# Kernel tuning notes

Hardware: AMD Instinct MI355X
Metric: run time of the kernel (lower is better)

## Reference

```python
import jax, jax.numpy as jnp
import numpy as np

B, N, H = 4096, 64, 256

def setup_inputs() -> dict:
    key = jax.random.key(0)
    ks = jax.random.split(key, 6)
    scale = 1.0 / np.sqrt(H)
    return {
        "s_t": jax.random.normal(ks[0], (B, H), dtype=jnp.float32),
        "h": jax.random.normal(ks[1], (1, N, H), dtype=jnp.float32) * scale,
        "w": jax.random.normal(ks[2], (1, N, H), dtype=jnp.float32) * scale,
        "U_w": jax.random.normal(ks[3], (H, H), dtype=jnp.float32) * scale,
        "V_w": jax.random.normal(ks[4], (H, H), dtype=jnp.float32) * scale,
        "W_w": jax.random.normal(ks[5], (H, H), dtype=jnp.float32) * scale,
        "prelu_a": jnp.full((1,), 0.25, dtype=jnp.float32),
    }

def _prelu(x, a):
    return jnp.where(x >= 0, x, a * x)

def reference(s_t, h, w, U_w, V_w, W_w, prelu_a):
    # gate: (h + w) @ s_t^T  -> [B, N]
    g = jax.nn.sigmoid(jnp.einsum('onh,bh->bn', h + w, s_t))[..., None]  # [B,N,1]
    # candidate: U(h) + V(w) + W(s_t), broadcast [1,N,H] + [B,1,H] -> [B,N,H]
    cand = _prelu(
        jnp.einsum('onh,kh->onk', h, U_w)
        + jnp.einsum('onh,kh->onk', w, V_w)
        + (s_t @ W_w.T)[:, None, :],
        prelu_a,
    )
    h_new = h + g * cand  # [B,N,H]
    h_new = h_new / jnp.linalg.norm(h_new, axis=2, keepdims=True)
    return h_new
```

## Files before the change

kernel.cpp:

```cpp
#include <hip/hip_runtime.h>
#include <hip/hip_bf16.h>

#define BATCH 4096
#define NMEM  64
#define HDIM  256
#define MROWS 320

typedef __attribute__((ext_vector_type(8))) short short8;
typedef __attribute__((ext_vector_type(4))) float floatx4;

__device__ __forceinline__ float bf2f(unsigned short u) {
    union { unsigned int i; float f; } v; v.i = ((unsigned int)u) << 16; return v.f;
}
__device__ __forceinline__ unsigned short f2bf(float f) {
    union { float f; unsigned int i; } v; v.f = f;
    unsigned int x = v.i;
    return (unsigned short)((x + 0x7FFFu + ((x >> 16) & 1u)) >> 16);
}
__device__ __forceinline__ short8 pack_bf16x8(float4 f0, float4 f1) {
    short8 a;
    a[0] = (short)f2bf(f0.x); a[1] = (short)f2bf(f0.y);
    a[2] = (short)f2bf(f0.z); a[3] = (short)f2bf(f0.w);
    a[4] = (short)f2bf(f1.x); a[5] = (short)f2bf(f1.y);
    a[6] = (short)f2bf(f1.z); a[7] = (short)f2bf(f1.w);
    return a;
}

__global__ __launch_bounds__(256) void prep_kernel(
    const float* __restrict__ h,
    const float* __restrict__ w,
    const float* __restrict__ U_w,
    const float* __restrict__ V_w,
    const float* __restrict__ W_w,
    unsigned short* __restrict__ M,
    unsigned short* __restrict__ A)
{
    const int bid = blockIdx.x;
    const int t   = threadIdx.x;
    if (bid < 16) {
        const int wv   = t >> 6;
        const int lane = t & 63;
        const int m = lane & 15;
        const int q = lane >> 4;
        const int j0 = bid * 16;

        const float* ah = h   + (size_t)(wv * 16 + m) * HDIM;
        const float* aw = w   + (size_t)(wv * 16 + m) * HDIM;
        const float* bu = U_w + (size_t)(j0 + m) * HDIM;
        const float* bv = V_w + (size_t)(j0 + m) * HDIM;

        floatx4 acc = {0.f, 0.f, 0.f, 0.f};
        #pragma unroll
        for (int ks = 0; ks < 16; ++ks) {
            const float* asrc = (ks < 8) ? ah : aw;
            const float* bsrc = (ks < 8) ? bu : bv;
            const int off = (ks & 7) * 32 + q * 8;
            float4 a0 = *(const float4*)(asrc + off);
            float4 a1 = *(const float4*)(asrc + off + 4);
            float4 b0 = *(const float4*)(bsrc + off);
            float4 b1 = *(const float4*)(bsrc + off + 4);
            acc = __builtin_amdgcn_mfma_f32_16x16x32_bf16(
                pack_bf16x8(a0, a1), pack_bf16x8(b0, b1), acc, 0, 0, 0);
        }
        #pragma unroll
        for (int r = 0; r < 4; ++r)
            A[(size_t)(wv * 16 + q * 4 + r) * HDIM + j0 + m] = f2bf(acc[r]);
    } else {
        const int r0 = (bid - 16) * 20;
        for (int rr = 0; rr < 20; ++rr) {
            const int r = r0 + rr;
            float v;
            if (r < 256) v = W_w[(size_t)r * HDIM + t];
            else         v = h[(size_t)(r - 256) * HDIM + t] + w[(size_t)(r - 256) * HDIM + t];
            M[(size_t)r * HDIM + t] = f2bf(v);
        }
    }
}

__global__ __launch_bounds__(256) void gemm_kernel(
    const float* __restrict__ s_t,
    const unsigned short* __restrict__ M,
    float* __restrict__ Call)
{
    const int b0   = blockIdx.x * 16;
    const int wave = threadIdx.x >> 6;
    const int lane = threadIdx.x & 63;
    const int m = lane & 15;
    const int q = lane >> 4;

    const float* arow = s_t + (size_t)(b0 + m) * HDIM;
    short8 afrag[8];
    #pragma unroll
    for (int ks = 0; ks < 8; ++ks) {
        const int base = ks * 32 + q * 8;
        afrag[ks] = pack_bf16x8(*(const float4*)(arow + base),
                                *(const float4*)(arow + base + 4));
    }

    #pragma unroll
    for (int jt = 0; jt < 5; ++jt) {
        const int j0 = (wave + jt * 4) * 16;
        const short8* brow = (const short8*)(M + (size_t)(j0 + m) * HDIM);
        floatx4 acc = {0.f, 0.f, 0.f, 0.f};
        #pragma unroll
        for (int ks = 0; ks < 8; ++ks) {
            short8 bfrag = brow[ks * 4 + q];
            acc = __builtin_amdgcn_mfma_f32_16x16x32_bf16(afrag[ks], bfrag, acc, 0, 0, 0);
        }
        #pragma unroll
        for (int r = 0; r < 4; ++r)
            Call[(size_t)(b0 + q * 4 + r) * MROWS + j0 + m] = acc[r];
    }
}

__global__ __launch_bounds__(256) void fuse_kernel(
    const float* __restrict__ h,
    const unsigned short* __restrict__ A,
    const float* __restrict__ Call,
    const float* __restrict__ prelu_a,
    float* __restrict__ out)
{
    __shared__ float C_lds[HDIM];
    __shared__ float g_lds[NMEM];

    const int t = threadIdx.x;
    const int b = blockIdx.x;
    const float pa = prelu_a[0];

    C_lds[t] = Call[(size_t)b * MROWS + t];
    if (t < NMEM) {
        float x = Call[(size_t)b * MROWS + 256 + t];
        g_lds[t] = 1.f / (1.f + __expf(-x));
    }
    __syncthreads();

    const int wave = t >> 6;
    const int lane = t & 63;
    const int qw   = lane >> 4;
    const int lq   = lane & 15;

    #pragma unroll
    for (int i = 0; i < 4; ++i) {
        const int n = i * 16 + wave * 4 + qw;
        const float g = g_lds[n];
        const float* hrow = h + (size_t)n * HDIM;
        const unsigned short* Arow = A + (size_t)n * HDIM;

        float y[16];
        float ss = 0.f;
        #pragma unroll
        for (int j = 0; j < 4; ++j) {
            const int k = lq * 4 + j * 64;
            float4  hv = *(const float4*)(hrow + k);
            ushort4 av = *(const ushort4*)(Arow + k);
            float4  cv = *(const float4*)(&C_lds[k]);
            float x0 = bf2f(av.x) + cv.x;
            float x1 = bf2f(av.y) + cv.y;
            float x2 = bf2f(av.z) + cv.z;
            float x3 = bf2f(av.w) + cv.w;
            x0 = (x0 >= 0.f) ? x0 : pa * x0;
            x1 = (x1 >= 0.f) ? x1 : pa * x1;
            x2 = (x2 >= 0.f) ? x2 : pa * x2;
            x3 = (x3 >= 0.f) ? x3 : pa * x3;
            float y0 = hv.x + g * x0;
            float y1 = hv.y + g * x1;
            float y2 = hv.z + g * x2;
            float y3 = hv.w + g * x3;
            y[j * 4 + 0] = y0; y[j * 4 + 1] = y1;
            y[j * 4 + 2] = y2; y[j * 4 + 3] = y3;
            ss += y0 * y0 + y1 * y1 + y2 * y2 + y3 * y3;
        }
        ss += __shfl_xor(ss, 1);
        ss += __shfl_xor(ss, 2);
        ss += __shfl_xor(ss, 4);
        ss += __shfl_xor(ss, 8);
        const float rn = rsqrtf(ss);

        float* orow = out + ((size_t)b * NMEM + n) * HDIM;
        #pragma unroll
        for (int j = 0; j < 4; ++j) {
            const int k = lq * 4 + j * 64;
            float4 ov;
            ov.x = y[j * 4 + 0] * rn;
            ov.y = y[j * 4 + 1] * rn;
            ov.z = y[j * 4 + 2] * rn;
            ov.w = y[j * 4 + 3] * rn;
            *(float4*)(orow + k) = ov;
        }
    }
}

extern "C" void kernel_launch(void* const* d_in, const int* in_sizes, int n_in,
                              void* d_out, int out_size, void* d_ws, size_t ws_size,
                              hipStream_t stream) {
    const float* s_t     = (const float*)d_in[0];
    const float* h       = (const float*)d_in[1];
    const float* w       = (const float*)d_in[2];
    const float* U_w     = (const float*)d_in[3];
    const float* V_w     = (const float*)d_in[4];
    const float* W_w     = (const float*)d_in[5];
    const float* prelu_a = (const float*)d_in[6];
    float* out = (float*)d_out;

    unsigned short* M = (unsigned short*)d_ws;
    unsigned short* A = (unsigned short*)((char*)d_ws + MROWS * HDIM * 2);
    float* Call = (float*)((char*)d_ws + MROWS * HDIM * 2 + NMEM * HDIM * 2);

    prep_kernel<<<32, 256, 0, stream>>>(h, w, U_w, V_w, W_w, M, A);
    gemm_kernel<<<BATCH / 16, 256, 0, stream>>>(s_t, M, Call);
    fuse_kernel<<<BATCH, 256, 0, stream>>>(h, A, Call, prelu_a, out);
}
```

Before: 300.3 us.

## Fuse batch GEMM with gating/normalize epilogue, tiling over batch and memory slots

Merges the s_t GEMM and the elementwise gate/PReLU/normalize kernel into one kernel. Each block computes C and gate for 16 batch rows into LDS, then processes 16 memory slots with h and A rows held in registers across the batch rows. This removes the global Call intermediate and a launch, and stops h/A being reloaded per batch row. The price is that the C GEMM is recomputed once per slot-group (4x redundant MFMA work) and LDS usage rises.

```diff
diff --git a/kernel.cpp b/kernel.cpp
--- a/kernel.cpp
+++ b/kernel.cpp
@@ -77,14 +77,22 @@
     }
 }
 
-__global__ __launch_bounds__(256) void gemm_kernel(
+__global__ __launch_bounds__(256, 4) void fused_kernel(
     const float* __restrict__ s_t,
+    const float* __restrict__ h,
     const unsigned short* __restrict__ M,
-    float* __restrict__ Call)
+    const unsigned short* __restrict__ A,
+    const float* __restrict__ prelu_a,
+    float* __restrict__ out)
 {
-    const int b0   = blockIdx.x * 16;
-    const int wave = threadIdx.x >> 6;
-    const int lane = threadIdx.x & 63;
+    __shared__ float C_lds[16][HDIM];
+    __shared__ float g_lds[16][16];
+
+    const int b0 = (blockIdx.x >> 2) * 16;
+    const int n0 = (blockIdx.x & 3) * 16;
+    const int t    = threadIdx.x;
+    const int wave = t >> 6;
+    const int lane = t & 63;
     const int m = lane & 15;
     const int q = lane >> 4;
 
@@ -96,76 +104,71 @@
         afrag[ks] = pack_bf16x8(*(const float4*)(arow + base),
                                 *(const float4*)(arow + base + 4));
     }
-
     #pragma unroll
-    for (int jt = 0; jt < 5; ++jt) {
-        const int j0 = (wave + jt * 4) * 16;
+    for (int i = 0; i < 4; ++i) {
+        const int j0 = (wave * 4 + i) * 16;
         const short8* brow = (const short8*)(M + (size_t)(j0 + m) * HDIM);
         floatx4 acc = {0.f, 0.f, 0.f, 0.f};
         #pragma unroll
-        for (int ks = 0; ks < 8; ++ks) {
-            short8 bfrag = brow[ks * 4 + q];
-            acc = __builtin_amdgcn_mfma_f32_16x16x32_bf16(afrag[ks], bfrag, acc, 0, 0, 0);
-        }
+        for (int ks = 0; ks < 8; ++ks)
+            acc = __builtin_amdgcn_mfma_f32_16x16x32_bf16(
+                afrag[ks], brow[ks * 4 + q], acc, 0, 0, 0);
         #pragma unroll
         for (int r = 0; r < 4; ++r)
-            Call[(size_t)(b0 + q * 4 + r) * MROWS + j0 + m] = acc[r];
-    }
-}
-
-__global__ __launch_bounds__(256) void fuse_kernel(
-    const float* __restrict__ h,
-    const unsigned short* __restrict__ A,
-    const float* __restrict__ Call,
-    const float* __restrict__ prelu_a,
-    float* __restrict__ out)
-{
-    __shared__ float C_lds[HDIM];
-    __shared__ float g_lds[NMEM];
-
-    const int t = threadIdx.x;
-    const int b = blockIdx.x;
+            C_lds[q * 4 + r][j0 + m] = acc[r];
+    }
+    if (wave == 3) {
+        const short8* brow = (const short8*)(M + (size_t)(256 + n0 + m) * HDIM);
+        floatx4 acc = {0.f, 0.f, 0.f, 0.f};
+        #pragma unroll
+        for (int ks = 0; ks < 8; ++ks)
+            acc = __builtin_amdgcn_mfma_f32_16x16x32_bf16(
+                afrag[ks], brow[ks * 4 + q], acc, 0, 0, 0);
+        #pragma unroll
+        for (int r = 0; r < 4; ++r)
+            g_lds[q * 4 + r][m] = 1.f / (1.f + __expf(-acc[r]));
+    }
+    __syncthreads();
+
     const float pa = prelu_a[0];
-
-    C_lds[t] = Call[(size_t)b * MROWS + t];
-    if (t < NMEM) {
-        float x = Call[(size_t)b * MROWS + 256 + t];
-        g_lds[t] = 1.f / (1.f + __expf(-x));
-    }
-    __syncthreads();
-
-    const int wave = t >> 6;
-    const int lane = t & 63;
-    const int qw   = lane >> 4;
-    const int lq   = lane & 15;
-
+    const int nl = wave * 4 + q;
+    const int n  = n0 + nl;
+    const float* hrow = h + (size_t)n * HDIM;
+    const unsigned short* Arow = A + (size_t)n * HDIM;
+
+    float hv[16], av[16];
     #pragma unroll
-    for (int i = 0; i < 4; ++i) {
-        const int n = i * 16 + wave * 4 + qw;
-        const float g = g_lds[n];
-        const float* hrow = h + (size_t)n * HDIM;
-        const unsigned short* Arow = A + (size_t)n * HDIM;
-
+    for (int j = 0; j < 4; ++j) {
+        const int k = m * 4 + j * 64;
+        float4  h4 = *(const float4*)(hrow + k);
+        ushort4 a4 = *(const ushort4*)(Arow + k);
+        hv[j * 4 + 0] = h4.x; hv[j * 4 + 1] = h4.y;
+        hv[j * 4 + 2] = h4.z; hv[j * 4 + 3] = h4.w;
+        av[j * 4 + 0] = bf2f(a4.x); av[j * 4 + 1] = bf2f(a4.y);
+        av[j * 4 + 2] = bf2f(a4.z); av[j * 4 + 3] = bf2f(a4.w);
+    }
+
+    #pragma unroll 2
+    for (int b = 0; b < 16; ++b) {
+        const float g = g_lds[b][nl];
         float y[16];
         float ss = 0.f;
         #pragma unroll
         for (int j = 0; j < 4; ++j) {
-            const int k = lq * 4 + j * 64;
-            float4  hv = *(const float4*)(hrow + k);
-            ushort4 av = *(const ushort4*)(Arow + k);
-            float4  cv = *(const float4*)(&C_lds[k]);
-            float x0 = bf2f(av.x) + cv.x;
-            float x1 = bf2f(av.y) + cv.y;
-            float x2 = bf2f(av.z) + cv.z;
-            float x3 = bf2f(av.w) + cv.w;
+            const int k = m * 4 + j * 64;
+            float4 cv = *(const float4*)(&C_lds[b][k]);
+            float x0 = av[j * 4 + 0] + cv.x;
+            float x1 = av[j * 4 + 1] + cv.y;
+            float x2 = av[j * 4 + 2] + cv.z;
+            float x3 = av[j * 4 + 3] + cv.w;
             x0 = (x0 >= 0.f) ? x0 : pa * x0;
             x1 = (x1 >= 0.f) ? x1 : pa * x1;
             x2 = (x2 >= 0.f) ? x2 : pa * x2;
             x3 = (x3 >= 0.f) ? x3 : pa * x3;
-            float y0 = hv.x + g * x0;
-            float y1 = hv.y + g * x1;
-            float y2 = hv.z + g * x2;
-            float y3 = hv.w + g * x3;
+            float y0 = hv[j * 4 + 0] + g * x0;
+            float y1 = hv[j * 4 + 1] + g * x1;
+            float y2 = hv[j * 4 + 2] + g * x2;
+            float y3 = hv[j * 4 + 3] + g * x3;
             y[j * 4 + 0] = y0; y[j * 4 + 1] = y1;
             y[j * 4 + 2] = y2; y[j * 4 + 3] = y3;
             ss += y0 * y0 + y1 * y1 + y2 * y2 + y3 * y3;
@@ -176,16 +179,15 @@
         ss += __shfl_xor(ss, 8);
         const float rn = rsqrtf(ss);
 
-        float* orow = out + ((size_t)b * NMEM + n) * HDIM;
+        float* orow = out + ((size_t)(b0 + b) * NMEM + n) * HDIM;
         #pragma unroll
         for (int j = 0; j < 4; ++j) {
-            const int k = lq * 4 + j * 64;
             float4 ov;
             ov.x = y[j * 4 + 0] * rn;
             ov.y = y[j * 4 + 1] * rn;
             ov.z = y[j * 4 + 2] * rn;
             ov.w = y[j * 4 + 3] * rn;
-            *(float4*)(orow + k) = ov;
+            *(float4*)(orow + m * 4 + j * 64) = ov;
         }
     }
 }
@@ -204,9 +206,7 @@
 
     unsigned short* M = (unsigned short*)d_ws;
     unsigned short* A = (unsigned short*)((char*)d_ws + MROWS * HDIM * 2);
-    float* Call = (float*)((char*)d_ws + MROWS * HDIM * 2 + NMEM * HDIM * 2);
 
     prep_kernel<<<32, 256, 0, stream>>>(h, w, U_w, V_w, W_w, M, A);
-    gemm_kernel<<<BATCH / 16, 256, 0, stream>>>(s_t, M, Call);
-    fuse_kernel<<<BATCH, 256, 0, stream>>>(h, A, Call, prelu_a, out);
-}
+    fused_kernel<<<(BATCH / 16) * 4, 256, 0, stream>>>(s_t, h, M, A, prelu_a, out);
+}
```

Result: no change. 294.6 us (-1.9%).
